# Performance work log

Hardware: AMD Instinct MI355X
Metric: run time of the kernel (lower is better)

## Reference

```python
import jax, jax.numpy as jnp
import numpy as np

D_MODEL = 3072
N_HEADS = 24
HEAD_DIM = D_MODEL // N_HEADS          # 128
Q_PROJ = D_MODEL // 2                  # 1536
KV_PROJ = 2 * D_MODEL // 3             # 2048
ROPE_DIM = HEAD_DIM // 2               # 64 (qk_rope_dim == qk_no_rope_dim)
MAX_LEN = 2048
ROPE_THETA = 10000.0
EPS = 1e-6
B, S = 2, 2048


def setup_inputs() -> dict:
    key = jax.random.key(0)
    ks = jax.random.split(key, 7)
    return {
        "x": jax.random.normal(ks[0], (B, S, D_MODEL), dtype=jnp.float32),
        "scale": jnp.ones((D_MODEL,), dtype=jnp.float32),
        "w_dq": 0.01 * jax.random.normal(ks[1], (D_MODEL, Q_PROJ), dtype=jnp.float32),
        "w_uq": 0.01 * jax.random.normal(ks[2], (Q_PROJ, D_MODEL), dtype=jnp.float32),
        "w_dkv": 0.01 * jax.random.normal(ks[3], (D_MODEL, KV_PROJ + ROPE_DIM), dtype=jnp.float32),
        "w_ukv": 0.01 * jax.random.normal(ks[4], (KV_PROJ, D_MODEL + N_HEADS * ROPE_DIM), dtype=jnp.float32),
        "w_o": 0.01 * jax.random.normal(ks[5], (D_MODEL, D_MODEL), dtype=jnp.float32),
    }


def _rope_cos_sin(seq_len):
    # freqs over full head_dim, sliced to rope_dim//2 then tiled x2 (as in torch repeat)
    freqs = 1.0 / (ROPE_THETA ** (jnp.arange(0, HEAD_DIM, 2, dtype=jnp.float32) / HEAD_DIM))
    angles = jnp.arange(seq_len, dtype=jnp.float32)[:, None] * freqs[None, :]  # [S, 64]
    ang = angles[:, : ROPE_DIM // 2]                                            # [S, 32]
    cos = jnp.tile(jnp.cos(ang), (1, 2))                                        # [S, 64]
    sin = jnp.tile(jnp.sin(ang), (1, 2))
    return cos[None, None], sin[None, None]  # [1,1,S,64]


def _rotate_half(t):
    a, b = jnp.split(t, 2, axis=-1)
    return jnp.concatenate([-b, a], axis=-1)


def reference(x, scale, w_dq, w_uq, w_dkv, w_ukv, w_o):
    b, s, _ = x.shape
    # RMSNorm pre-normalization
    xn = scale * (x * jax.lax.rsqrt(jnp.mean(x * x, axis=-1, keepdims=True) + EPS))
    # two-stage query projection
    q = (xn @ w_dq) @ w_uq                                   # [B,S,D]
    q = q.reshape(b, s, N_HEADS, HEAD_DIM).transpose(0, 2, 1, 3)  # [B,H,S,hd]
    q_no_rope, q_rope = jnp.split(q, [ROPE_DIM], axis=-1)
    cos, sin = _rope_cos_sin(s)
    q_rope = q_rope * cos + _rotate_half(q_rope) * sin
    # KV down projection (this is the kv cache)
    kv_down = xn @ w_dkv                                     # [B,S,KV_PROJ+rope]
    kv_no_rope, k_rope = jnp.split(kv_down, [KV_PROJ], axis=-1)
    # KV up projection
    kv_up = kv_no_rope @ w_ukv                               # [B,S,H*(hd+rope)]
    kv_up = kv_up.reshape(b, s, N_HEADS, HEAD_DIM + ROPE_DIM).transpose(0, 2, 1, 3)
    key, value = jnp.split(kv_up, [ROPE_DIM], axis=-1)       # key [B,H,S,64], value [B,H,S,128]
    # shared rope key (one head, broadcast to all heads)
    k_rope = k_rope[:, None, :, :]                           # [B,1,S,64]
    k_rope = k_rope * cos + _rotate_half(k_rope) * sin
    k_rope = jnp.broadcast_to(k_rope, (b, N_HEADS, s, ROPE_DIM))
    final_q = jnp.concatenate([q_no_rope, q_rope], axis=-1)  # [B,H,S,128]
    final_k = jnp.concatenate([key, k_rope], axis=-1)        # [B,H,S,128]
    # masked SDPA (causal, past_length=0)
    inv_scale = 1.0 / jnp.sqrt(jnp.asarray(HEAD_DIM, dtype=x.dtype))
    scores = jnp.einsum("bhsd,bhtd->bhst", final_q, final_k) * inv_scale
    causal = jnp.tril(jnp.ones((s, s), dtype=bool))
    scores = jnp.where(causal[None, None], scores, jnp.asarray(-1e30, dtype=scores.dtype))
    attn = jax.nn.softmax(scores, axis=-1)
    attn_out = jnp.einsum("bhst,bhtd->bhsd", attn, value)    # [B,H,S,128]
    attn_out = attn_out.transpose(0, 2, 1, 3).reshape(b, s, D_MODEL)
    output = attn_out @ w_o.T
    return output, kv_down
```

## Files before the change

### kernel.cpp

```cpp
#include <hip/hip_runtime.h>
#include <hip/hip_bf16.h>
#include <stdint.h>

using bf16_t = __bf16;
using bf16x8 = __attribute__((ext_vector_type(8))) __bf16;
using bf16x4 = __attribute__((ext_vector_type(4))) __bf16;
using f32x4  = __attribute__((ext_vector_type(4))) float;

#define D_MODEL 3072
#define N_HEADS 24
#define HEAD_DIM 128
#define Q_PROJ 1536
#define KV_PROJ 2048
#define ROPE_DIM 64
#define S_LEN 2048
#define NTOK 4096
#define KVDN 2112
#define KVUN 4608

__device__ __forceinline__ void async_ld16(const void* g, void* l) {
    __builtin_amdgcn_global_load_lds(
        (__attribute__((address_space(1))) uint32_t*)(uintptr_t)g,
        (__attribute__((address_space(3))) uint32_t*)(uint32_t)(uintptr_t)l,
        16, 0, 0);
}

#define BARRIER() __builtin_amdgcn_s_barrier()
#define WAITV0() asm volatile("s_waitcnt vmcnt(0)" ::: "memory")

__global__ __launch_bounds__(256) void rmsnorm_kernel(
    const float* __restrict__ x, const float* __restrict__ sc, bf16_t* __restrict__ xn)
{
    const int tok = blockIdx.x;
    const int t = threadIdx.x;
    const float4* xr = (const float4*)(x + (size_t)tok * D_MODEL);
    float4 a = xr[t], b = xr[t + 256], c = xr[t + 512];
    float ss = a.x*a.x + a.y*a.y + a.z*a.z + a.w*a.w
             + b.x*b.x + b.y*b.y + b.z*b.z + b.w*b.w
             + c.x*c.x + c.y*c.y + c.z*c.z + c.w*c.w;
    #pragma unroll
    for (int off = 32; off >= 1; off >>= 1) ss += __shfl_xor(ss, off);
    __shared__ float red[4];
    if ((t & 63) == 0) red[t >> 6] = ss;
    __syncthreads();
    const float inv = rsqrtf((red[0] + red[1] + red[2] + red[3]) * (1.0f / D_MODEL) + 1e-6f);
    const float4* sr = (const float4*)sc;
    float4 s0 = sr[t], s1 = sr[t + 256], s2 = sr[t + 512];
    bf16x4* xo = (bf16x4*)(xn + (size_t)tok * D_MODEL);
    bf16x4 o;
    o[0]=(bf16_t)(a.x*s0.x*inv); o[1]=(bf16_t)(a.y*s0.y*inv); o[2]=(bf16_t)(a.z*s0.z*inv); o[3]=(bf16_t)(a.w*s0.w*inv);
    xo[t] = o;
    o[0]=(bf16_t)(b.x*s1.x*inv); o[1]=(bf16_t)(b.y*s1.y*inv); o[2]=(bf16_t)(b.z*s1.z*inv); o[3]=(bf16_t)(b.w*s1.w*inv);
    xo[t + 256] = o;
    o[0]=(bf16_t)(c.x*s2.x*inv); o[1]=(bf16_t)(c.y*s2.y*inv); o[2]=(bf16_t)(c.z*s2.z*inv); o[3]=(bf16_t)(c.w*s2.w*inv);
    xo[t + 512] = o;
}

__global__ void transpose_conv(const float* __restrict__ in, bf16_t* __restrict__ out, int K, int N)
{
    __shared__ float tile[32][33];
    const int n0 = blockIdx.x * 32, k0 = blockIdx.y * 32;
    const int tx = threadIdx.x, ty = threadIdx.y;
    #pragma unroll
    for (int i = 0; i < 32; i += 8)
        tile[ty + i][tx] = in[(size_t)(k0 + ty + i) * N + n0 + tx];
    __syncthreads();
    #pragma unroll
    for (int i = 0; i < 32; i += 8)
        out[(size_t)(n0 + ty + i) * K + k0 + tx] = (bf16_t)tile[tx][ty + i];
}

__global__ void conv_bf16(const float* __restrict__ in, bf16_t* __restrict__ out, int n4)
{
    const int stride = gridDim.x * 256;
    for (int i = blockIdx.x * 256 + threadIdx.x; i < n4; i += stride) {
        float4 v = ((const float4*)in)[i];
        bf16x4 o;
        o[0] = (bf16_t)v.x; o[1] = (bf16_t)v.y; o[2] = (bf16_t)v.z; o[3] = (bf16_t)v.w;
        ((bf16x4*)out)[i] = o;
    }
}

template<int RH>
__device__ __forceinline__ void mfma16(f32x4 (&acc)[8][4], const bf16x8 (&af)[4],
                                       const bf16x8 (&bfv)[4]) {
    __builtin_amdgcn_s_setprio(1);
    #pragma unroll
    for (int i = 0; i < 4; ++i)
        #pragma unroll
        for (int cf = 0; cf < 4; ++cf)
            acc[RH*4+i][cf] = __builtin_amdgcn_mfma_f32_16x16x32_bf16(af[i], bfv[cf], acc[RH*4+i][cf], 0, 0, 0);
    __builtin_amdgcn_s_setprio(0);
}

__global__ __launch_bounds__(512, 2) void gemm256(
    const bf16_t* __restrict__ A, const bf16_t* __restrict__ B, int N, int K,
    float* __restrict__ Cf, int ldf, int flo, int fhi,
    bf16_t* __restrict__ Cb1, int ldb1, int b1lo, int b1hi,
    bf16_t* __restrict__ Cb2, int ldb2, int b2lo, int b2hi)
{
    __shared__ char LDS[131072];
    char* Lc = LDS;
    const int tid = threadIdx.x;
    const int wv = tid >> 6, lane = tid & 63;
    const int fr = lane & 15, fg = lane >> 4;
    const int wr = wv >> 2, wc = wv & 3;

    int lin = blockIdx.y * gridDim.x + blockIdx.x;
    const int nwg = gridDim.x * gridDim.y;
    if ((nwg & 7) == 0) lin = (lin & 7) * (nwg >> 3) + (lin >> 3);
    const int bx = lin % gridDim.x, by = lin / gridDim.x;
    const int m0 = by << 8, n0 = bx << 8;

    const uint32_t slot4 = (uint32_t)((fg ^ ((fr >> 1) & 3)) << 4);

    int grow[2], gcol[2];
    const bf16_t* agp[2]; const bf16_t* bgp[2];
    uint32_t aoff[2], boff[2];
    #pragma unroll
    for (int j = 0; j < 2; ++j) {
        const int c = j * 512 + tid;
        const int g = c ^ ((c >> 3) & 3);
        grow[j] = g >> 2; gcol[j] = g & 3;
        agp[j] = A + (size_t)(m0 + grow[j]) * K + gcol[j] * 8;
        int br = n0 + grow[j]; if (br > N - 1) br = N - 1;
        bgp[j] = B + (size_t)br * K + gcol[j] * 8;
        aoff[j] = (uint32_t)((j * 8 + wv) * 1024);
        boff[j] = (uint32_t)(65536 + (j * 8 + wv) * 1024);
    }

    f32x4 acc[8][4];
    f32x4 zero = {0.f, 0.f, 0.f, 0.f};
    #pragma unroll
    for (int i = 0; i < 8; ++i)
        #pragma unroll
        for (int j = 0; j < 4; ++j) acc[i][j] = zero;

    bf16x8 A0[4], A1[4], B0[4], B1[4];
    const int rowA = (wr << 7) + fr;
    const int rowB = (wc << 6) + fr;

    auto stA = [&](int t, int kh) {
        const uint32_t sb = (uint32_t)(((2*t + kh) & 3) << 14);
        #pragma unroll
        for (int j = 0; j < 2; ++j)
            async_ld16(agp[j] + t * 64 + kh * 32, Lc + sb + aoff[j]);
    };
    auto stB = [&](int t, int kh) {
        const uint32_t sb = (uint32_t)(((2*t + kh) & 3) << 14);
        #pragma unroll
        for (int j = 0; j < 2; ++j)
            async_ld16(bgp[j] + t * 64 + kh * 32, Lc + sb + boff[j]);
    };
    auto ldA4 = [&](int t, int kh, int rh, bf16x8 (&dst)[4]) {
        const uint32_t base = (uint32_t)(((2*t + kh) & 3) << 14);
        #pragma unroll
        for (int i = 0; i < 4; ++i)
            dst[i] = *(const bf16x8*)(Lc + base + (rowA + (rh * 4 + i) * 16) * 64 + slot4);
    };
    auto ldB4 = [&](int t, int kh, bf16x8 (&dst)[4]) {
        const uint32_t base = (uint32_t)(65536 + (((2*t + kh) & 3) << 14));
        #pragma unroll
        for (int cf = 0; cf < 4; ++cf)
            dst[cf] = *(const bf16x8*)(Lc + base + (rowB + cf * 16) * 64 + slot4);
    };

    const int NT = K >> 6;
    stA(0, 0); stB(0, 0); stA(0, 1); stB(0, 1);
    WAITV0(); BARRIER();
    ldA4(0, 0, 0, A0); ldB4(0, 0, B0);

    for (int t = 0; t < NT; ++t) {
        const bool pref = (t < NT - 1);
        ldA4(t, 0, 1, A1);
        if (pref) { stA(t + 1, 0); stB(t + 1, 0); }
        mfma16<0>(acc, A0, B0);
        BARRIER();
        ldA4(t, 1, 0, A0); ldB4(t, 1, B1);
        if (pref) { stA(t + 1, 1); stB(t + 1, 1); }
        mfma16<1>(acc, A1, B0);
        BARRIER();
        ldA4(t, 1, 1, A1);
        mfma16<0>(acc, A0, B1);
        if (pref) WAITV0();
        BARRIER();
        if (pref) { ldA4(t + 1, 0, 0, A0); ldB4(t + 1, 0, B0); }
        mfma16<1>(acc, A1, B1);
        BARRIER();
    }

    const int colb = n0 + (wc << 6) + fr;
    const int rowb = m0 + (wr << 7) + fg * 4;
    #pragma unroll
    for (int rf = 0; rf < 8; ++rf)
        #pragma unroll
        for (int cf = 0; cf < 4; ++cf) {
            const int col = colb + cf * 16;
            #pragma unroll
            for (int r = 0; r < 4; ++r) {
                const int row = rowb + rf * 16 + r;
                const float v = acc[rf][cf][r];
                if (Cf  && col >= flo  && col < fhi)  Cf [(size_t)row * ldf  + col - flo]  = v;
                if (Cb1 && col >= b1lo && col < b1hi) Cb1[(size_t)row * ldb1 + col - b1lo] = (bf16_t)v;
                if (Cb2 && col >= b2lo && col < b2hi) Cb2[(size_t)row * ldb2 + col - b2lo] = (bf16_t)v;
            }
        }
}

__global__ void rope_tab(float* __restrict__ ctab, float* __restrict__ stab)
{
    const int idx = blockIdx.x * 256 + threadIdx.x;
    if (idx >= S_LEN * 32) return;
    const int s = idx >> 5, i = idx & 31;
    const float freq = powf(10000.0f, -(float)(2 * i) * (1.0f / 128.0f));
    const float ang = (float)s * freq;
    ctab[idx] = cosf(ang);
    stab[idx] = sinf(ang);
}

__global__ void rope_q_kernel(bf16_t* __restrict__ q, const float* __restrict__ ctab,
                              const float* __restrict__ stab)
{
    const int idx = blockIdx.x * 256 + threadIdx.x;
    if (idx >= NTOK * N_HEADS * 32) return;
    const int i = idx & 31;
    const int rest = idx >> 5;
    const int h = rest % N_HEADS;
    const int tok = rest / N_HEADS;
    const int s = tok & (S_LEN - 1);
    bf16_t* p = q + (size_t)tok * D_MODEL + h * HEAD_DIM + 64;
    const float a = (float)p[i], b = (float)p[i + 32];
    const float c = ctab[s * 32 + i], sn = stab[s * 32 + i];
    p[i]      = (bf16_t)(a * c - b * sn);
    p[i + 32] = (bf16_t)(b * c + a * sn);
}

__global__ void rope_k_kernel(const float* __restrict__ kvd, bf16_t* __restrict__ kr,
                              const float* __restrict__ ctab, const float* __restrict__ stab)
{
    const int idx = blockIdx.x * 256 + threadIdx.x;
    if (idx >= NTOK * 32) return;
    const int i = idx & 31;
    const int tok = idx >> 5;
    const int s = tok & (S_LEN - 1);
    const float* p = kvd + (size_t)tok * KVDN + KV_PROJ;
    const float a = p[i], b = p[i + 32];
    const float c = ctab[s * 32 + i], sn = stab[s * 32 + i];
    kr[(size_t)tok * 64 + i]      = (bf16_t)(a * c - b * sn);
    kr[(size_t)tok * 64 + i + 32] = (bf16_t)(b * c + a * sn);
}

__global__ void vt_asm(const bf16_t* __restrict__ kvup, bf16_t* __restrict__ vt)
{
    __shared__ bf16_t tile[32][33];
    const int s0 = blockIdx.x * 32, d0 = blockIdx.y * 32, bh = blockIdx.z;
    const int b = bh / N_HEADS, h = bh % N_HEADS;
    const int tx = threadIdx.x, ty = threadIdx.y;
    #pragma unroll
    for (int i = 0; i < 32; i += 8)
        tile[ty + i][tx] = kvup[(size_t)(b * S_LEN + s0 + ty + i) * KVUN + h * 192 + 64 + d0 + tx];
    __syncthreads();
    #pragma unroll
    for (int i = 0; i < 32; i += 8)
        vt[((size_t)bh * HEAD_DIM + d0 + ty + i) * S_LEN + s0 + tx] = tile[tx][ty + i];
}

__global__ __launch_bounds__(256, 2) void attn_fwd(
    const bf16_t* __restrict__ Q, const bf16_t* __restrict__ KVUP,
    const bf16_t* __restrict__ KR, const bf16_t* __restrict__ VT,
    bf16_t* __restrict__ AO)
{
    __shared__ bf16_t Knr[2][64 * 64];
    __shared__ bf16_t Krp[2][64 * 64];
    __shared__ bf16_t Vls[2][128 * 64];

    const int bh = blockIdx.y;
    const int b = bh / N_HEADS, h = bh % N_HEADS;
    const int wave = threadIdx.x >> 6, lane = threadIdx.x & 63;
    const int fr = lane & 15, fg = lane >> 4;
    const int rx = fr & 7;
    const int hi = fg >> 1;
    const int s0l = fr + 32 * (fg & 1);
    const int s1l = s0l + 16;

    const bf16_t* Kb  = KVUP + (size_t)b * S_LEN * KVUN + (size_t)h * 192;
    const bf16_t* KRb = KR + (size_t)b * S_LEN * 64;
    const bf16_t* Vb  = VT + (size_t)bh * HEAD_DIM * S_LEN;

    const int srow   = lane >> 3;
    const int schunk = (lane & 7) ^ srow;
    const float l2e_isc = 0.127500625f;

    f32x4 zero = {0.f, 0.f, 0.f, 0.f};

    #pragma unroll 1
    for (int tp = 0; tp < 2; ++tp) {
        const int qt = (tp == 0) ? blockIdx.x : (15 - blockIdx.x);
        const int qb = qt * 128;
        const int wrow0 = qb + wave * 32;

        bf16x8 qf[2][4];
        #pragma unroll
        for (int rf = 0; rf < 2; ++rf)
            #pragma unroll
            for (int kc = 0; kc < 4; ++kc)
                qf[rf][kc] = *(const bf16x8*)(Q + (size_t)(b * S_LEN + wrow0 + rf * 16 + fr) * D_MODEL
                                              + h * HEAD_DIM + kc * 32 + fg * 8);
        f32x4 oacc[2][8];
        float m_i[2], l_i[2];
        #pragma unroll
        for (int rf = 0; rf < 2; ++rf) {
            #pragma unroll
            for (int nf = 0; nf < 8; ++nf) oacc[rf][nf] = zero;
            m_i[rf] = -1e30f; l_i[rf] = 0.f;
        }

        auto stage = [&](int kvb, int bf) {
            #pragma unroll
            for (int c = 0; c < 2; ++c) {
                const int r0 = wave * 16 + c * 8;
                async_ld16(Kb  + (size_t)(kvb + r0 + srow) * KVUN + schunk * 8, &Knr[bf][r0 * 64]);
                async_ld16(KRb + (size_t)(kvb + r0 + srow) * 64   + schunk * 8, &Krp[bf][r0 * 64]);
            }
            #pragma unroll
            for (int c = 0; c < 4; ++c) {
                const int r0 = wave * 32 + c * 8;
                async_ld16(Vb + (size_t)(r0 + srow) * S_LEN + kvb + schunk * 8, &Vls[bf][r0 * 64]);
            }
        };

        const int kvend = qb + 128;
        int cur = 0;
        stage(0, 0);
        __syncthreads();

        #pragma unroll 1
        for (int kvb = 0; kvb < kvend; kvb += 64) {
            if (kvb + 64 < kvend) stage(kvb + 64, cur ^ 1);

            if (kvb <= wrow0 + 31) {
                const bf16_t* Kc = Knr[cur];
                const bf16_t* Rc = Krp[cur];
                const bf16_t* Vc = Vls[cur];

                f32x4 sacc[2][4];
                #pragma unroll
                for (int rf = 0; rf < 2; ++rf)
                    #pragma unroll
                    for (int jn = 0; jn < 4; ++jn) sacc[rf][jn] = zero;
                __builtin_amdgcn_s_setprio(1);
                #pragma unroll
                for (int jn = 0; jn < 4; ++jn) {
                    const int krow = jn * 16 + fr;
                    bf16x8 kA = *(const bf16x8*)(Kc + krow * 64 + (((0 + fg) ^ rx) << 3));
                    bf16x8 kB = *(const bf16x8*)(Kc + krow * 64 + (((4 + fg) ^ rx) << 3));
                    bf16x8 kC = *(const bf16x8*)(Rc + krow * 64 + (((0 + fg) ^ rx) << 3));
                    bf16x8 kD = *(const bf16x8*)(Rc + krow * 64 + (((4 + fg) ^ rx) << 3));
                    #pragma unroll
                    for (int rf = 0; rf < 2; ++rf) {
                        sacc[rf][jn] = __builtin_amdgcn_mfma_f32_16x16x32_bf16(kA, qf[rf][0], sacc[rf][jn], 0, 0, 0);
                        sacc[rf][jn] = __builtin_amdgcn_mfma_f32_16x16x32_bf16(kB, qf[rf][1], sacc[rf][jn], 0, 0, 0);
                        sacc[rf][jn] = __builtin_amdgcn_mfma_f32_16x16x32_bf16(kC, qf[rf][2], sacc[rf][jn], 0, 0, 0);
                        sacc[rf][jn] = __builtin_amdgcn_mfma_f32_16x16x32_bf16(kD, qf[rf][3], sacc[rf][jn], 0, 0, 0);
                    }
                }
                __builtin_amdgcn_s_setprio(0);

                const bool needMask = (kvb + 63 > wrow0);
                uint32_t pk[2][4][2];
                float scf[2];
                #pragma unroll
                for (int rf = 0; rf < 2; ++rf) {
                    const int qrow = wrow0 + rf * 16 + fr;
                    float mx = -1e30f;
                    #pragma unroll
                    for (int jn = 0; jn < 4; ++jn)
                        #pragma unroll
                        for (int r = 0; r < 4; ++r) {
                            float v = sacc[rf][jn][r] * l2e_isc;
                            if (needMask && (kvb + jn * 16 + fg * 4 + r > qrow)) v = -1e30f;
                            sacc[rf][jn][r] = v;
                            mx = fmaxf(mx, v);
                        }
                    mx = fmaxf(mx, __shfl_xor(mx, 16));
                    mx = fmaxf(mx, __shfl_xor(mx, 32));
                    const float mn = fmaxf(m_i[rf], mx);
                    scf[rf] = __builtin_amdgcn_exp2f(m_i[rf] - mn);
                    m_i[rf] = mn;
                    float ls = 0.f;
                    #pragma unroll
                    for (int jn = 0; jn < 4; ++jn) {
                        float p0 = __builtin_amdgcn_exp2f(sacc[rf][jn][0] - mn);
                        float p1 = __builtin_amdgcn_exp2f(sacc[rf][jn][1] - mn);
                        float p2 = __builtin_amdgcn_exp2f(sacc[rf][jn][2] - mn);
                        float p3 = __builtin_amdgcn_exp2f(sacc[rf][jn][3] - mn);
                        ls += (p0 + p1) + (p2 + p3);
                        union { bf16x4 h; uint32_t w[2]; } cv;
                        cv.h[0] = (bf16_t)p0; cv.h[1] = (bf16_t)p1;
                        cv.h[2] = (bf16_t)p2; cv.h[3] = (bf16_t)p3;
                        pk[rf][jn][0] = cv.w[0]; pk[rf][jn][1] = cv.w[1];
                    }
                    ls += __shfl_xor(ls, 16);
                    ls += __shfl_xor(ls, 32);
                    l_i[rf] = l_i[rf] * scf[rf] + ls;
                    #pragma unroll
                    for (int nf = 0; nf < 8; ++nf)
                        #pragma unroll
                        for (int r = 0; r < 4; ++r) oacc[rf][nf][r] *= scf[rf];
                }

                bf16x8 bfr[2][2];
                #pragma unroll
                for (int rf = 0; rf < 2; ++rf)
                    #pragma unroll
                    for (int ks = 0; ks < 2; ++ks) {
                        const uint32_t t00 = __shfl(pk[rf][2*ks][0],   s0l);
                        const uint32_t t01 = __shfl(pk[rf][2*ks][1],   s0l);
                        const uint32_t t10 = __shfl(pk[rf][2*ks+1][0], s0l);
                        const uint32_t t11 = __shfl(pk[rf][2*ks+1][1], s0l);
                        const uint32_t u00 = __shfl(pk[rf][2*ks][0],   s1l);
                        const uint32_t u01 = __shfl(pk[rf][2*ks][1],   s1l);
                        const uint32_t u10 = __shfl(pk[rf][2*ks+1][0], s1l);
                        const uint32_t u11 = __shfl(pk[rf][2*ks+1][1], s1l);
                        union { bf16x8 h; uint32_t w[4]; } bb;
                        bb.w[0] = hi ? t10 : t00;
                        bb.w[1] = hi ? t11 : t01;
                        bb.w[2] = hi ? u10 : u00;
                        bb.w[3] = hi ? u11 : u01;
                        bfr[rf][ks] = bb.h;
                    }

                __builtin_amdgcn_s_setprio(1);
                #pragma unroll
                for (int nf = 0; nf < 8; ++nf) {
                    const int vrow = nf * 16 + fr;
                    bf16x8 v0 = *(const bf16x8*)(Vc + vrow * 64 + (((0 + fg) ^ rx) << 3));
                    bf16x8 v1 = *(const bf16x8*)(Vc + vrow * 64 + (((4 + fg) ^ rx) << 3));
                    #pragma unroll
                    for (int rf = 0; rf < 2; ++rf) {
                        oacc[rf][nf] = __builtin_amdgcn_mfma_f32_16x16x32_bf16(v0, bfr[rf][0], oacc[rf][nf], 0, 0, 0);
                        oacc[rf][nf] = __builtin_amdgcn_mfma_f32_16x16x32_bf16(v1, bfr[rf][1], oacc[rf][nf], 0, 0, 0);
                    }
                }
                __builtin_amdgcn_s_setprio(0);
            }
            __syncthreads();
            cur ^= 1;
        }

        #pragma unroll
        for (int rf = 0; rf < 2; ++rf) {
            const float rl = __builtin_amdgcn_rcpf(l_i[rf]);
            const int qrow = wrow0 + rf * 16 + fr;
            bf16_t* aob = AO + (size_t)(b * S_LEN + qrow) * D_MODEL + h * HEAD_DIM + fg * 4;
            #pragma unroll
            for (int nf = 0; nf < 8; ++nf) {
                bf16x4 o;
                o[0] = (bf16_t)(oacc[rf][nf][0] * rl);
                o[1] = (bf16_t)(oacc[rf][nf][1] * rl);
                o[2] = (bf16_t)(oacc[rf][nf][2] * rl);
                o[3] = (bf16_t)(oacc[rf][nf][3] * rl);
                *(bf16x4*)(aob + nf * 16) = o;
            }
        }
    }
}

extern "C" void kernel_launch(void* const* d_in, const int* in_sizes, int n_in,
                              void* d_out, int out_size, void* d_ws, size_t ws_size,
                              hipStream_t stream)
{
    const float* x     = (const float*)d_in[0];
    const float* scale = (const float*)d_in[1];
    const float* w_dq  = (const float*)d_in[2];
    const float* w_uq  = (const float*)d_in[3];
    const float* w_dkv = (const float*)d_in[4];
    const float* w_ukv = (const float*)d_in[5];
    const float* w_o   = (const float*)d_in[6];
    float* out0 = (float*)d_out;
    float* out1 = out0 + (size_t)NTOK * D_MODEL;

    if (ws_size < 187039744ull) return;
    char* ws = (char*)d_ws;
    bf16_t* XN    = (bf16_t*)(ws + 0);
    bf16_t* WCAT  = (bf16_t*)(ws + 25165824ull);
    bf16_t* WUQT  = (bf16_t*)(ws + 47579136ull);
    bf16_t* WUKVT = (bf16_t*)(ws + 57016320ull);
    bf16_t* WOB   = (bf16_t*)(ws + 75890688ull);
    bf16_t* QD    = (bf16_t*)(ws + 94765056ull);
    bf16_t* Qb    = (bf16_t*)(ws + 107347968ull);
    bf16_t* KVNR  = (bf16_t*)(ws + 132513792ull);
    bf16_t* KVUP  = (bf16_t*)(ws + 149291008ull);
    bf16_t* KRB   = (bf16_t*)(ws + 94765056ull);
    float*  CTAB  = (float*) (ws + 95289344ull);
    float*  STAB  = (float*) (ws + 95551488ull);
    bf16_t* VTb   = WCAT;
    bf16_t* AO    = XN;

    rmsnorm_kernel<<<NTOK, 256, 0, stream>>>(x, scale, XN);
    transpose_conv<<<dim3(1536/32, 3072/32), dim3(32,8), 0, stream>>>(w_dq,  WCAT, 3072, 1536);
    transpose_conv<<<dim3(2112/32, 3072/32), dim3(32,8), 0, stream>>>(w_dkv, WCAT + (size_t)1536*3072, 3072, 2112);
    transpose_conv<<<dim3(3072/32, 1536/32), dim3(32,8), 0, stream>>>(w_uq,  WUQT, 1536, 3072);
    transpose_conv<<<dim3(4608/32, 2048/32), dim3(32,8), 0, stream>>>(w_ukv, WUKVT, 2048, 4608);
    conv_bf16<<<2048, 256, 0, stream>>>(w_o, WOB, (D_MODEL * D_MODEL) / 4);

    gemm256<<<dim3(15, 16), 512, 0, stream>>>(XN, WCAT, 3648, 3072,
        out1, KVDN, 1536, 3648,
        QD,   Q_PROJ, 0, 1536,
        KVNR, KV_PROJ, 1536, 3584);
    gemm256<<<dim3(12, 16), 512, 0, stream>>>(QD, WUQT, 3072, 1536,
        nullptr, 0, 0, 0, Qb, D_MODEL, 0, 3072, nullptr, 0, 0, 0);
    rope_tab<<<(S_LEN * 32 + 255) / 256, 256, 0, stream>>>(CTAB, STAB);
    rope_q_kernel<<<(NTOK * N_HEADS * 32 + 255) / 256, 256, 0, stream>>>(Qb, CTAB, STAB);
    rope_k_kernel<<<(NTOK * 32 + 255) / 256, 256, 0, stream>>>(out1, KRB, CTAB, STAB);
    gemm256<<<dim3(18, 16), 512, 0, stream>>>(KVNR, WUKVT, 4608, 2048,
        nullptr, 0, 0, 0, KVUP, KVUN, 0, 4608, nullptr, 0, 0, 0);
    vt_asm<<<dim3(S_LEN/32, HEAD_DIM/32, 48), dim3(32,8), 0, stream>>>(KVUP, VTb);
    attn_fwd<<<dim3(8, 48), 256, 0, stream>>>(Qb, KVUP, KRB, VTb, AO);
    gemm256<<<dim3(12, 16), 512, 0, stream>>>(AO, WOB, 3072, 3072,
        out0, D_MODEL, 0, 3072, nullptr, 0, 0, 0, nullptr, 0, 0, 0);
}
```

Measured before the change: 570.2 us.

## Template GEMM N-tile width and fuse V transpose into KV-up GEMM epilogue

```diff
diff --git a/kernel.cpp b/kernel.cpp
--- a/kernel.cpp
+++ b/kernel.cpp
@@ -81,25 +81,29 @@
     }
 }
 
-template<int RH>
-__device__ __forceinline__ void mfma16(f32x4 (&acc)[8][4], const bf16x8 (&af)[4],
-                                       const bf16x8 (&bfv)[4]) {
+template<int RH, int BNF>
+__device__ __forceinline__ void mfmaQ(f32x4 (&acc)[8][BNF], const bf16x8 (&af)[4],
+                                      const bf16x8 (&bfv)[BNF]) {
     __builtin_amdgcn_s_setprio(1);
     #pragma unroll
     for (int i = 0; i < 4; ++i)
         #pragma unroll
-        for (int cf = 0; cf < 4; ++cf)
+        for (int cf = 0; cf < BNF; ++cf)
             acc[RH*4+i][cf] = __builtin_amdgcn_mfma_f32_16x16x32_bf16(af[i], bfv[cf], acc[RH*4+i][cf], 0, 0, 0);
     __builtin_amdgcn_s_setprio(0);
 }
 
+template<int BNF>
 __global__ __launch_bounds__(512, 2) void gemm256(
     const bf16_t* __restrict__ A, const bf16_t* __restrict__ B, int N, int K,
     float* __restrict__ Cf, int ldf, int flo, int fhi,
     bf16_t* __restrict__ Cb1, int ldb1, int b1lo, int b1hi,
-    bf16_t* __restrict__ Cb2, int ldb2, int b2lo, int b2hi)
-{
-    __shared__ char LDS[131072];
+    bf16_t* __restrict__ Cb2, int ldb2, int b2lo, int b2hi,
+    bf16_t* __restrict__ vt)
+{
+    constexpr int BN = BNF * 64;
+    constexpr uint32_t BSLOT = BNF * 4096;
+    __shared__ char LDS[65536 + 4 * BSLOT];
     char* Lc = LDS;
     const int tid = threadIdx.x;
     const int wv = tid >> 6, lane = tid & 63;
@@ -110,35 +114,35 @@
     const int nwg = gridDim.x * gridDim.y;
     if ((nwg & 7) == 0) lin = (lin & 7) * (nwg >> 3) + (lin >> 3);
     const int bx = lin % gridDim.x, by = lin / gridDim.x;
-    const int m0 = by << 8, n0 = bx << 8;
+    const int m0 = by << 8, n0 = bx * BN;
 
     const uint32_t slot4 = (uint32_t)((fg ^ ((fr >> 1) & 3)) << 4);
 
-    int grow[2], gcol[2];
     const bf16_t* agp[2]; const bf16_t* bgp[2];
     uint32_t aoff[2], boff[2];
     #pragma unroll
     for (int j = 0; j < 2; ++j) {
         const int c = j * 512 + tid;
         const int g = c ^ ((c >> 3) & 3);
-        grow[j] = g >> 2; gcol[j] = g & 3;
-        agp[j] = A + (size_t)(m0 + grow[j]) * K + gcol[j] * 8;
-        int br = n0 + grow[j]; if (br > N - 1) br = N - 1;
-        bgp[j] = B + (size_t)br * K + gcol[j] * 8;
+        agp[j] = A + (size_t)(m0 + (g >> 2)) * K + (g & 3) * 8;
         aoff[j] = (uint32_t)((j * 8 + wv) * 1024);
-        boff[j] = (uint32_t)(65536 + (j * 8 + wv) * 1024);
+        const int cb = j * (BNF * 128) + tid;
+        const int gb = cb ^ ((cb >> 3) & 3);
+        int br = n0 + (gb >> 2); if (br > N - 1) br = N - 1;
+        bgp[j] = B + (size_t)br * K + (gb & 3) * 8;
+        boff[j] = (uint32_t)(j * (BNF * 2048) + wv * 1024);
     }
 
-    f32x4 acc[8][4];
+    f32x4 acc[8][BNF];
     f32x4 zero = {0.f, 0.f, 0.f, 0.f};
     #pragma unroll
     for (int i = 0; i < 8; ++i)
         #pragma unroll
-        for (int j = 0; j < 4; ++j) acc[i][j] = zero;
-
-    bf16x8 A0[4], A1[4], B0[4], B1[4];
+        for (int j = 0; j < BNF; ++j) acc[i][j] = zero;
+
+    bf16x8 A0[4], A1[4], B0[BNF], B1[BNF];
     const int rowA = (wr << 7) + fr;
-    const int rowB = (wc << 6) + fr;
+    const int rowB = wc * (BNF * 16) + fr;
 
     auto stA = [&](int t, int kh) {
         const uint32_t sb = (uint32_t)(((2*t + kh) & 3) << 14);
@@ -147,10 +151,12 @@
             async_ld16(agp[j] + t * 64 + kh * 32, Lc + sb + aoff[j]);
     };
     auto stB = [&](int t, int kh) {
-        const uint32_t sb = (uint32_t)(((2*t + kh) & 3) << 14);
-        #pragma unroll
-        for (int j = 0; j < 2; ++j)
-            async_ld16(bgp[j] + t * 64 + kh * 32, Lc + sb + boff[j]);
+        const uint32_t sb = 65536u + (uint32_t)(((2*t + kh) & 3) * BSLOT);
+        if (tid < BNF * 128) {
+            #pragma unroll
+            for (int j = 0; j < 2; ++j)
+                async_ld16(bgp[j] + t * 64 + kh * 32, Lc + sb + boff[j]);
+        }
     };
     auto ldA4 = [&](int t, int kh, int rh, bf16x8 (&dst)[4]) {
         const uint32_t base = (uint32_t)(((2*t + kh) & 3) << 14);
@@ -158,53 +164,79 @@
         for (int i = 0; i < 4; ++i)
             dst[i] = *(const bf16x8*)(Lc + base + (rowA + (rh * 4 + i) * 16) * 64 + slot4);
     };
-    auto ldB4 = [&](int t, int kh, bf16x8 (&dst)[4]) {
-        const uint32_t base = (uint32_t)(65536 + (((2*t + kh) & 3) << 14));
-        #pragma unroll
-        for (int cf = 0; cf < 4; ++cf)
+    auto ldBn = [&](int t, int kh, bf16x8 (&dst)[BNF]) {
+        const uint32_t base = 65536u + (uint32_t)(((2*t + kh) & 3) * BSLOT);
+        #pragma unroll
+        for (int cf = 0; cf < BNF; ++cf)
             dst[cf] = *(const bf16x8*)(Lc + base + (rowB + cf * 16) * 64 + slot4);
     };
 
     const int NT = K >> 6;
     stA(0, 0); stB(0, 0); stA(0, 1); stB(0, 1);
     WAITV0(); BARRIER();
-    ldA4(0, 0, 0, A0); ldB4(0, 0, B0);
+    ldA4(0, 0, 0, A0); ldBn(0, 0, B0);
 
     for (int t = 0; t < NT; ++t) {
         const bool pref = (t < NT - 1);
         ldA4(t, 0, 1, A1);
         if (pref) { stA(t + 1, 0); stB(t + 1, 0); }
-        mfma16<0>(acc, A0, B0);
+        mfmaQ<0, BNF>(acc, A0, B0);
         BARRIER();
-        ldA4(t, 1, 0, A0); ldB4(t, 1, B1);
+        ldA4(t, 1, 0, A0); ldBn(t, 1, B1);
         if (pref) { stA(t + 1, 1); stB(t + 1, 1); }
-        mfma16<1>(acc, A1, B0);
+        mfmaQ<1, BNF>(acc, A1, B0);
         BARRIER();
         ldA4(t, 1, 1, A1);
-        mfma16<0>(acc, A0, B1);
+        mfmaQ<0, BNF>(acc, A0, B1);
         if (pref) WAITV0();
         BARRIER();
-        if (pref) { ldA4(t + 1, 0, 0, A0); ldB4(t + 1, 0, B0); }
-        mfma16<1>(acc, A1, B1);
+        if (pref) { ldA4(t + 1, 0, 0, A0); ldBn(t + 1, 0, B0); }
+        mfmaQ<1, BNF>(acc, A1, B1);
         BARRIER();
     }
 
-    const int colb = n0 + (wc << 6) + fr;
+    const int colb = n0 + wc * (BNF * 16) + fr;
     const int rowb = m0 + (wr << 7) + fg * 4;
-    #pragma unroll
-    for (int rf = 0; rf < 8; ++rf)
-        #pragma unroll
-        for (int cf = 0; cf < 4; ++cf) {
-            const int col = colb + cf * 16;
-            #pragma unroll
-            for (int r = 0; r < 4; ++r) {
-                const int row = rowb + rf * 16 + r;
-                const float v = acc[rf][cf][r];
-                if (Cf  && col >= flo  && col < fhi)  Cf [(size_t)row * ldf  + col - flo]  = v;
-                if (Cb1 && col >= b1lo && col < b1hi) Cb1[(size_t)row * ldb1 + col - b1lo] = (bf16_t)v;
-                if (Cb2 && col >= b2lo && col < b2hi) Cb2[(size_t)row * ldb2 + col - b2lo] = (bf16_t)v;
+    if (vt) {
+        #pragma unroll
+        for (int rf = 0; rf < 8; ++rf) {
+            const int row0 = rowb + rf * 16;
+            const int bb = row0 >> 11, s0 = row0 & 2047;
+            #pragma unroll
+            for (int cf = 0; cf < BNF; ++cf) {
+                const int col = colb + cf * 16;
+                const int h = col / 192;
+                const int dm = col - h * 192;
+                if (dm < 64) {
+                    #pragma unroll
+                    for (int r = 0; r < 4; ++r)
+                        Cb1[(size_t)(row0 + r) * ldb1 + col] = (bf16_t)acc[rf][cf][r];
+                } else {
+                    bf16x4 o;
+                    o[0] = (bf16_t)acc[rf][cf][0];
+                    o[1] = (bf16_t)acc[rf][cf][1];
+                    o[2] = (bf16_t)acc[rf][cf][2];
+                    o[3] = (bf16_t)acc[rf][cf][3];
+                    *(bf16x4*)(vt + ((size_t)((bb * 24 + h) * 128 + dm - 64)) * 2048 + s0) = o;
+                }
             }
         }
+    } else {
+        #pragma unroll
+        for (int rf = 0; rf < 8; ++rf)
+            #pragma unroll
+            for (int cf = 0; cf < BNF; ++cf) {
+                const int col = colb + cf * 16;
+                #pragma unroll
+                for (int r = 0; r < 4; ++r) {
+                    const int row = rowb + rf * 16 + r;
+                    const float v = acc[rf][cf][r];
+                    if (Cf  && col >= flo  && col < fhi)  Cf [(size_t)row * ldf  + col - flo]  = v;
+                    if (Cb1 && col >= b1lo && col < b1hi) Cb1[(size_t)row * ldb1 + col - b1lo] = (bf16_t)v;
+                    if (Cb2 && col >= b2lo && col < b2hi) Cb2[(size_t)row * ldb2 + col - b2lo] = (bf16_t)v;
+                }
+            }
+    }
 }
 
 __global__ void rope_tab(float* __restrict__ ctab, float* __restrict__ stab)
@@ -248,21 +280,6 @@
     const float c = ctab[s * 32 + i], sn = stab[s * 32 + i];
     kr[(size_t)tok * 64 + i]      = (bf16_t)(a * c - b * sn);
     kr[(size_t)tok * 64 + i + 32] = (bf16_t)(b * c + a * sn);
-}
-
-__global__ void vt_asm(const bf16_t* __restrict__ kvup, bf16_t* __restrict__ vt)
-{
-    __shared__ bf16_t tile[32][33];
-    const int s0 = blockIdx.x * 32, d0 = blockIdx.y * 32, bh = blockIdx.z;
-    const int b = bh / N_HEADS, h = bh % N_HEADS;
-    const int tx = threadIdx.x, ty = threadIdx.y;
-    #pragma unroll
-    for (int i = 0; i < 32; i += 8)
-        tile[ty + i][tx] = kvup[(size_t)(b * S_LEN + s0 + ty + i) * KVUN + h * 192 + 64 + d0 + tx];
-    __syncthreads();
-    #pragma unroll
-    for (int i = 0; i < 32; i += 8)
-        vt[((size_t)bh * HEAD_DIM + d0 + ty + i) * S_LEN + s0 + tx] = tile[tx][ty + i];
 }
 
 __global__ __launch_bounds__(256, 2) void attn_fwd(
@@ -504,19 +521,18 @@
     transpose_conv<<<dim3(4608/32, 2048/32), dim3(32,8), 0, stream>>>(w_ukv, WUKVT, 2048, 4608);
     conv_bf16<<<2048, 256, 0, stream>>>(w_o, WOB, (D_MODEL * D_MODEL) / 4);
 
-    gemm256<<<dim3(15, 16), 512, 0, stream>>>(XN, WCAT, 3648, 3072,
+    gemm256<4><<<dim3(15, 16), 512, 0, stream>>>(XN, WCAT, 3648, 3072,
         out1, KVDN, 1536, 3648,
         QD,   Q_PROJ, 0, 1536,
-        KVNR, KV_PROJ, 1536, 3584);
-    gemm256<<<dim3(12, 16), 512, 0, stream>>>(QD, WUQT, 3072, 1536,
-        nullptr, 0, 0, 0, Qb, D_MODEL, 0, 3072, nullptr, 0, 0, 0);
+        KVNR, KV_PROJ, 1536, 3584, nullptr);
+    gemm256<3><<<dim3(16, 16), 512, 0, stream>>>(QD, WUQT, 3072, 1536,
+        nullptr, 0, 0, 0, Qb, D_MODEL, 0, 3072, nullptr, 0, 0, 0, nullptr);
     rope_tab<<<(S_LEN * 32 + 255) / 256, 256, 0, stream>>>(CTAB, STAB);
     rope_q_kernel<<<(NTOK * N_HEADS * 32 + 255) / 256, 256, 0, stream>>>(Qb, CTAB, STAB);
     rope_k_kernel<<<(NTOK * 32 + 255) / 256, 256, 0, stream>>>(out1, KRB, CTAB, STAB);
-    gemm256<<<dim3(18, 16), 512, 0, stream>>>(KVNR, WUKVT, 4608, 2048,
-        nullptr, 0, 0, 0, KVUP, KVUN, 0, 4608, nullptr, 0, 0, 0);
-    vt_asm<<<dim3(S_LEN/32, HEAD_DIM/32, 48), dim3(32,8), 0, stream>>>(KVUP, VTb);
+    gemm256<3><<<dim3(24, 16), 512, 0, stream>>>(KVNR, WUKVT, 4608, 2048,
+        nullptr, 0, 0, 0, KVUP, KVUN, 0, 0, nullptr, 0, 0, 0, VTb);
     attn_fwd<<<dim3(8, 48), 256, 0, stream>>>(Qb, KVUP, KRB, VTb, AO);
-    gemm256<<<dim3(12, 16), 512, 0, stream>>>(AO, WOB, 3072, 3072,
-        out0, D_MODEL, 0, 3072, nullptr, 0, 0, 0, nullptr, 0, 0, 0);
-}
+    gemm256<3><<<dim3(16, 16), 512, 0, stream>>>(AO, WOB, 3072, 3072,
+        out0, D_MODEL, 0, 3072, nullptr, 0, 0, 0, nullptr, 0, 0, 0, nullptr);
+}
```

Result: faster. 537.6 us (-5.7%).
